# Kernel tuning notes

Measured on AMD Instinct MI355X. Metric: run time of the kernel, lower is better.

## Reference

```python
import jax, jax.numpy as jnp
import numpy as np

EPS = 1e-8
LAM = 1.0


def setup_inputs() -> dict:
    key = jax.random.key(0)
    k1, k2 = jax.random.split(key)
    B, H, W = 32, 512, 512
    output = jax.random.normal(k1, (B, 1, H, W), dtype=jnp.float32)
    target = jax.random.normal(k2, (B, 1, H, W), dtype=jnp.float32)
    return {"output": output, "target": target}


def _frc_loss(output, target):
    # squeeze channel dim: (B,1,H,W) -> (B,H,W)
    output = output[:, 0]
    target = target[:, 0]
    B, H, W = output.shape
    rnyquist = H // 2

    # radial index map (H,W): round(sqrt(fx^2 + fy^2)) in pixel-frequency units
    fx = jnp.fft.fftfreq(H, 1.0 / H)
    fy = jnp.fft.fftfreq(W, 1.0 / W)
    X, Y = jnp.meshgrid(fx, fy, indexing='ij')
    radial = jnp.round(jnp.sqrt(X ** 2 + Y ** 2)).astype(jnp.int32)
    # bins > rnyquist were ignored by the original loop -> dump into extra bin
    idx = jnp.where(radial > rnyquist, rnyquist + 1, radial).reshape(-1)  # (H*W,)

    F1 = jnp.fft.fft2(output, norm='forward')  # (B,H,W) complex
    F2 = jnp.fft.fft2(target, norm='forward')

    # per-pixel correlation terms, laid out (HW, B) for segment_sum over leading axis
    a = (F1.real * F2.real + F1.imag * F2.imag).reshape(B, -1).T
    b = (F1.imag * F2.real - F1.real * F2.imag).reshape(B, -1).T
    c1 = (F1.real ** 2 + F1.imag ** 2).reshape(B, -1).T
    c2 = (F2.real ** 2 + F2.imag ** 2).reshape(B, -1).T
    stacked = jnp.stack([a, b, c1, c2], axis=-1)  # (HW, B, 4)

    # single-pass radial-bin segment sum (replaces O(R*H*W) masked loop)
    sums = jax.ops.segment_sum(stacked, idx, num_segments=rnyquist + 2)
    sums = sums[:rnyquist + 1]  # drop overflow bin -> (rnyquist+1, B, 4)
    C_r, C_i, C1, C2 = sums[..., 0], sums[..., 1], sums[..., 2], sums[..., 3]

    frc = jnp.sqrt(C_r ** 2 + C_i ** 2) / (jnp.sqrt(C1 * C2) + EPS)
    return LAM * jnp.mean((1.0 - frc) ** 2)


def reference(output, target):
    return _frc_loss(output, target)
```

## Files before the change

### kernel.cpp

```cpp
#include <hip/hip_runtime.h>
#include <math.h>

#define NIMG 32
#define NB3  771
#define PI_F 3.14159265358979323846f

__device__ __forceinline__ float2 cadd(float2 a, float2 b){ return make_float2(a.x+b.x, a.y+b.y); }
__device__ __forceinline__ float2 csub(float2 a, float2 b){ return make_float2(a.x-b.x, a.y-b.y); }
__device__ __forceinline__ float2 cmul(float2 a, float2 b){ return make_float2(a.x*b.x - a.y*b.y, a.x*b.y + a.y*b.x); }
__device__ __forceinline__ float2 cmul_mi(float2 a){ return make_float2(a.y, -a.x); }
__device__ __forceinline__ float2 tw(const float2* T, int m){ return T[m + (m >> 3)]; }
__device__ __forceinline__ int   sw(int pos){ return pos + (pos >> 3); }

__device__ __forceinline__ void dft8(float2* x) {
    const float c = 0.70710678118654752f;
    float2 u0 = cadd(x[0], x[4]), u1 = cadd(x[1], x[5]);
    float2 u2 = cadd(x[2], x[6]), u3 = cadd(x[3], x[7]);
    float2 v0 = csub(x[0], x[4]);
    float2 d1 = csub(x[1], x[5]);
    float2 v1 = make_float2(c*(d1.x + d1.y), c*(d1.y - d1.x));
    float2 d2 = csub(x[2], x[6]);
    float2 v2 = make_float2(d2.y, -d2.x);
    float2 d3 = csub(x[3], x[7]);
    float2 v3 = make_float2(-c*(d3.x - d3.y), -c*(d3.x + d3.y));
    float2 e0 = cadd(u0,u2), e1 = cadd(u1,u3);
    float2 f0 = csub(u0,u2), f1 = cmul_mi(csub(u1,u3));
    float2 g0 = cadd(v0,v2), g1 = cadd(v1,v3);
    float2 h0 = csub(v0,v2), h1 = cmul_mi(csub(v1,v3));
    x[0] = cadd(e0,e1); x[4] = csub(e0,e1);
    x[2] = cadd(f0,f1); x[6] = csub(f0,f1);
    x[1] = cadd(g0,g1); x[5] = csub(g0,g1);
    x[3] = cadd(h0,h1); x[7] = csub(h0,h1);
}

__device__ __forceinline__ void wave_fft512_dual(float2* Xa, float2* Xb,
                                                 float2* Sw, const float2* T,
                                                 int J) {
    dft8(Xa);
    dft8(Xb);
#pragma unroll
    for (int k = 1; k < 8; ++k) Xa[k] = cmul(Xa[k], tw(T, J * k));
#pragma unroll
    for (int k = 1; k < 8; ++k) Xb[k] = cmul(Xb[k], tw(T, J * k));
    const int jj = J + (J >> 3);
    const int j2 = J & 7;
    const int bb = 72 * (J >> 3) + j2;

#pragma unroll
    for (int k = 0; k < 8; ++k) Sw[jj + 72*k] = Xa[k];
#pragma unroll
    for (int q = 0; q < 8; ++q) Xa[q] = Sw[bb + 9*q];
#pragma unroll
    for (int k = 0; k < 8; ++k) Sw[jj + 72*k] = Xb[k];
#pragma unroll
    for (int q = 0; q < 8; ++q) Xb[q] = Sw[bb + 9*q];

    dft8(Xa);
    dft8(Xb);
#pragma unroll
    for (int k = 1; k < 8; ++k) Xa[k] = cmul(Xa[k], tw(T, 8 * j2 * k));
#pragma unroll
    for (int k = 1; k < 8; ++k) Xb[k] = cmul(Xb[k], tw(T, 8 * j2 * k));

#pragma unroll
    for (int k = 0; k < 8; ++k) Sw[bb + 9*k] = Xa[k];
#pragma unroll
    for (int q = 0; q < 8; ++q) Xa[q] = Sw[9*J + q];
#pragma unroll
    for (int k = 0; k < 8; ++k) Sw[bb + 9*k] = Xb[k];
#pragma unroll
    for (int q = 0; q < 8; ++q) Xb[q] = Sw[9*J + q];

    dft8(Xa);
    dft8(Xb);
}

__global__ __launch_bounds__(256) void fft_rows_T(const float* __restrict__ xr,
                                                  const float* __restrict__ yr,
                                                  float2* __restrict__ Zt) {
    __shared__ float2 S[4 * 576];
    __shared__ float2 T[576];
    const int t = threadIdx.x, w = t >> 6, J = t & 63;
    const int im = blockIdx.x >> 6, grp = blockIdx.x & 63;

#pragma unroll
    for (int i = 0; i < 2; ++i) {
        const int m = t + 256 * i;
        float s, c;
        __sincosf(-2.0f * PI_F * (float)m / 512.0f, &s, &c);
        T[m + (m >> 3)] = make_float2(c, s);
    }

    const size_t b0 = ((size_t)(im * 512 + grp * 8 + w)) << 9;
    const size_t b1 = b0 + (4u << 9);
    float2 X0[8], X1[8];
#pragma unroll
    for (int q = 0; q < 8; ++q) {
        X0[q] = make_float2(xr[b0 + J + 64*q], yr[b0 + J + 64*q]);
        X1[q] = make_float2(xr[b1 + J + 64*q], yr[b1 + J + 64*q]);
    }
    __syncthreads();

    float2* Sw = S + w * 576;
    wave_fft512_dual(X0, X1, Sw, T, J);

    const int r = ((J & 7) << 3) | (J >> 3);

#pragma unroll
    for (int k = 0; k < 8; ++k) Sw[64*k + r] = X0[k];
    __syncthreads();
    float2 eA[4], eB[4];
#pragma unroll
    for (int j = 0; j < 4; ++j) { eA[j] = S[j*576 + t]; eB[j] = S[j*576 + t + 256]; }
    __syncthreads();

#pragma unroll
    for (int k = 0; k < 8; ++k) Sw[64*k + r] = X1[k];
    __syncthreads();

    const size_t zb = ((size_t)im << 18) + (grp << 3);
    {
        float4* o = (float4*)(Zt + zb + ((size_t)t << 9));
        float2 f0 = S[0*576 + t], f1 = S[1*576 + t];
        float2 f2 = S[2*576 + t], f3 = S[3*576 + t];
        o[0] = make_float4(eA[0].x, eA[0].y, eA[1].x, eA[1].y);
        o[1] = make_float4(eA[2].x, eA[2].y, eA[3].x, eA[3].y);
        o[2] = make_float4(f0.x, f0.y, f1.x, f1.y);
        o[3] = make_float4(f2.x, f2.y, f3.x, f3.y);
    }
    {
        float4* o = (float4*)(Zt + zb + ((size_t)(t + 256) << 9));
        float2 f0 = S[0*576 + t + 256], f1 = S[1*576 + t + 256];
        float2 f2 = S[2*576 + t + 256], f3 = S[3*576 + t + 256];
        o[0] = make_float4(eB[0].x, eB[0].y, eB[1].x, eB[1].y);
        o[1] = make_float4(eB[2].x, eB[2].y, eB[3].x, eB[3].y);
        o[2] = make_float4(f0.x, f0.y, f1.x, f1.y);
        o[3] = make_float4(f2.x, f2.y, f3.x, f3.y);
    }
}

__global__ __launch_bounds__(256) void fft_cols_rings(const float2* __restrict__ Zt,
                                                      float* __restrict__ sums,
                                                      int big) {
    __shared__ float2 S[4 * 576];
    __shared__ float2 T[576];
    __shared__ float  bins[258 * 3];
    const int t = threadIdx.x, w = t >> 6, J = t & 63;
    const int im = blockIdx.x >> 6, g = blockIdx.x & 63;
    const int p = 4 * g + w;

#pragma unroll
    for (int i = 0; i < 2; ++i) {
        const int m = t + 256 * i;
        float s, c;
        __sincosf(-2.0f * PI_F * (float)m / 512.0f, &s, &c);
        T[m + (m >> 3)] = make_float2(c, s);
    }
    for (int i = t; i < 258 * 3; i += 256) bins[i] = 0.0f;

    const int c0 = (p == 0) ? 0   : p;
    const int c1 = (p == 0) ? 256 : 512 - p;
    const float2* rp0 = Zt + ((size_t)im << 18) + ((size_t)c0 << 9);
    const float2* rp1 = Zt + ((size_t)im << 18) + ((size_t)c1 << 9);
    float2 X0[8], X1[8];
#pragma unroll
    for (int q = 0; q < 8; ++q) { X0[q] = rp0[J + 64*q]; X1[q] = rp1[J + 64*q]; }
    __syncthreads();

    float2* A = S + w * 576;
    const int r  = ((J & 7) << 3) | (J >> 3);
    const int pk = r + (r >> 3);

    const float scale = 1.0f / (512.0f * 512.0f);
    auto pix = [&](float2 zk, float2 zm, float& av, float& c1v, float& c2v) {
        float f1r = 0.5f * (zk.x + zm.x) * scale;
        float f1i = 0.5f * (zk.y - zm.y) * scale;
        float f2r = 0.5f * (zk.y + zm.y) * scale;
        float f2i = 0.5f * (zm.x - zk.x) * scale;
        av  = f1r * f2r + f1i * f2i;
        c1v = f1r * f1r + f1i * f1i;
        c2v = f2r * f2r + f2i * f2i;
    };
    auto flush = [&](int ring, float a, float b, float c) {
        if (ring >= 0 && ring <= 256) {
            unsafeAtomicAdd(&bins[ring*3+0], a);
            unsafeAtomicAdd(&bins[ring*3+1], b);
            unsafeAtomicAdd(&bins[ring*3+2], c);
        }
    };

    wave_fft512_dual(X0, X1, A, T, J);

#pragma unroll
    for (int k = 0; k < 8; ++k) A[72*k + pk] = X0[k];

    float2 asv[8];
    if (p == 0) {
        int cur0 = -1;
        float a0 = 0, b0 = 0, c0v = 0;
#pragma unroll
        for (int i = 0; i < 8; ++i) {
            const int ky  = 8*J + i;
            const int kyp = (512 - ky) & 511;
            float2 zk = A[sw(ky)], zm = A[sw(kyp)];
            const float fk = (ky < 256) ? (float)ky : (float)(ky - 512);
            float av, cv, dv;
            pix(zk, zm, av, cv, dv);
            int rr = (int)rintf(fabsf(fk)); if (rr > 256) rr = 257;
            if (rr != cur0) { flush(cur0, a0, b0, c0v); cur0 = rr; a0 = av; b0 = cv; c0v = dv; }
            else            { a0 += av; b0 += cv; c0v += dv; }
        }
        flush(cur0, a0, b0, c0v);
    } else {
#pragma unroll
        for (int i = 0; i < 8; ++i) asv[i] = A[9*J + i];
    }

#pragma unroll
    for (int k = 0; k < 8; ++k) A[72*k + pk] = X1[k];

    if (p == 0) {
        int cur1 = -1;
        float a1 = 0, b1 = 0, c1v = 0;
#pragma unroll
        for (int i = 0; i < 8; ++i) {
            const int ky  = 8*J + i;
            const int kyp = (512 - ky) & 511;
            float2 zk = A[sw(ky)], zm = A[sw(kyp)];
            const float fk = (ky < 256) ? (float)ky : (float)(ky - 512);
            float av, cv, dv;
            pix(zk, zm, av, cv, dv);
            int rr = (int)rintf(sqrtf(fk*fk + 65536.0f)); if (rr > 256) rr = 257;
            if (rr != cur1) { flush(cur1, a1, b1, c1v); cur1 = rr; a1 = av; b1 = cv; c1v = dv; }
            else            { a1 += av; b1 += cv; c1v += dv; }
        }
        flush(cur1, a1, b1, c1v);
    } else {
        const float fy2 = (float)p * (float)p;
        int curR = -1;
        float sA = 0, sB = 0, sC = 0;
#pragma unroll
        for (int i = 0; i < 8; ++i) {
            const int ky  = 8*J + i;
            const int kyp = (512 - ky) & 511;
            float2 zk = asv[i];
            float2 zm = A[sw(kyp)];
            float a1v, b1v, d1v, a2v, b2v, d2v;
            pix(zk, zm, a1v, b1v, d1v);
            pix(zm, zk, a2v, b2v, d2v);
            const float fk = (ky < 256) ? (float)ky : (float)(ky - 512);
            int rr = (int)rintf(sqrtf(fk*fk + fy2)); if (rr > 256) rr = 257;
            const float aa = a1v + a2v, bb = b1v + b2v, cc = d1v + d2v;
            if (rr != curR) { flush(curR, sA, sB, sC); curR = rr; sA = aa; sB = bb; sC = cc; }
            else            { sA += aa; sB += bb; sC += cc; }
        }
        flush(curR, sA, sB, sC);
    }
    __syncthreads();

    if (big) {
        float* dst = sums + (size_t)blockIdx.x * NB3;
        for (int i = t; i < NB3; i += 256) dst[i] = bins[i];
    } else {
        float* dst = sums + (size_t)(im * 8 + (g & 7)) * NB3;
        for (int i = t; i < NB3; i += 256) unsafeAtomicAdd(&dst[i], bins[i]);
    }
}

__global__ __launch_bounds__(256) void finalize(const float* __restrict__ sums,
                                                float* __restrict__ out, int spi) {
    const int b = blockIdx.x, t = threadIdx.x;
    float acc = 0.0f;
    for (int r = t; r < 257; r += 256) {
        float cr = 0.f, c1 = 0.f, c2 = 0.f;
        for (int s = 0; s < spi; ++s) {
            const float* pp = sums + (size_t)(b * spi + s) * NB3 + r * 3;
            cr += pp[0]; c1 += pp[1]; c2 += pp[2];
        }
        float frc = fabsf(cr) / (sqrtf(c1 * c2) + 1e-8f);
        float d = 1.0f - frc;
        acc += d * d;
    }
#pragma unroll
    for (int off = 32; off > 0; off >>= 1) acc += __shfl_down(acc, off);
    __shared__ float red[4];
    if ((t & 63) == 0) red[t >> 6] = acc;
    __syncthreads();
    if (t == 0)
        unsafeAtomicAdd(out, (red[0] + red[1] + red[2] + red[3]) *
                             (1.0f / (257.0f * (float)NIMG)));
}

extern "C" void kernel_launch(void* const* d_in, const int* in_sizes, int n_in,
                              void* d_out, int out_size, void* d_ws, size_t ws_size,
                              hipStream_t stream) {
    const float* xr = (const float*)d_in[0];
    const float* yr = (const float*)d_in[1];

    float2* Zt = (float2*)d_ws;
    const size_t ztBytes = ((size_t)NIMG << 18) * sizeof(float2);
    float* sums = (float*)((char*)d_ws + ztBytes);
    const int big = (ws_size >= ztBytes + (size_t)2048 * NB3 * sizeof(float)) ? 1 : 0;

    if (!big)
        hipMemsetAsync(sums, 0, (size_t)NIMG * 8 * NB3 * sizeof(float), stream);
    hipMemsetAsync(d_out, 0, sizeof(float), stream);

    fft_rows_T    <<<dim3(NIMG * 64), dim3(256), 0, stream>>>(xr, yr, Zt);
    fft_cols_rings<<<dim3(NIMG * 64), dim3(256), 0, stream>>>(Zt, sums, big);
    finalize      <<<dim3(NIMG), dim3(256), 0, stream>>>(sums, (float*)d_out, big ? 64 : 8);
}
```

Measured before the change: 207.3 us.

## Tile intermediate layout, fuse finalize via last-block reduction, drop memsets, use symmetry

The intermediate spectrum is now stored in 8-column tiles, so row-FFT stores and column-FFT loads use contiguous chunks instead of 4 KB-strided accesses. Zeroing of the partial sums and counter moves into the first kernel, which removes two memset launches. The finalize kernel is folded into the column kernel through an atomic counter, with the last block doing the final reduction. The mirrored pixel term is replaced by doubling the first, based on conjugate symmetry. Together these cut launch overhead and improve memory coalescing, at the cost of a serial tail reduction in one block and atomics on the partial sums.

```diff
diff --git a/kernel.cpp b/kernel.cpp
--- a/kernel.cpp
+++ b/kernel.cpp
@@ -3,6 +3,7 @@
 
 #define NIMG 32
 #define NB3  771
+#define NSLICE (NIMG * 8)
 #define PI_F 3.14159265358979323846f
 
 __device__ __forceinline__ float2 cadd(float2 a, float2 b){ return make_float2(a.x+b.x, a.y+b.y); }
@@ -77,11 +78,19 @@
 
 __global__ __launch_bounds__(256) void fft_rows_T(const float* __restrict__ xr,
                                                   const float* __restrict__ yr,
-                                                  float2* __restrict__ Zt) {
+                                                  float2* __restrict__ Zt,
+                                                  float* __restrict__ sums,
+                                                  unsigned int* __restrict__ counter) {
     __shared__ float2 S[4 * 576];
     __shared__ float2 T[576];
     const int t = threadIdx.x, w = t >> 6, J = t & 63;
     const int im = blockIdx.x >> 6, grp = blockIdx.x & 63;
+
+    if (blockIdx.x < NSLICE) {
+        float* z = sums + (size_t)blockIdx.x * NB3;
+        for (int i = t; i < NB3; i += 256) z[i] = 0.0f;
+        if (blockIdx.x == 0 && t == 0) *counter = 0u;
+    }
 
 #pragma unroll
     for (int i = 0; i < 2; ++i) {
@@ -118,9 +127,9 @@
     for (int k = 0; k < 8; ++k) Sw[64*k + r] = X1[k];
     __syncthreads();
 
-    const size_t zb = ((size_t)im << 18) + (grp << 3);
+    const size_t zb = ((size_t)im << 18) + ((size_t)grp << 12);
     {
-        float4* o = (float4*)(Zt + zb + ((size_t)t << 9));
+        float4* o = (float4*)(Zt + zb + ((size_t)t << 3));
         float2 f0 = S[0*576 + t], f1 = S[1*576 + t];
         float2 f2 = S[2*576 + t], f3 = S[3*576 + t];
         o[0] = make_float4(eA[0].x, eA[0].y, eA[1].x, eA[1].y);
@@ -129,7 +138,7 @@
         o[3] = make_float4(f2.x, f2.y, f3.x, f3.y);
     }
     {
-        float4* o = (float4*)(Zt + zb + ((size_t)(t + 256) << 9));
+        float4* o = (float4*)(Zt + zb + ((size_t)(t + 256) << 3));
         float2 f0 = S[0*576 + t + 256], f1 = S[1*576 + t + 256];
         float2 f2 = S[2*576 + t + 256], f3 = S[3*576 + t + 256];
         o[0] = make_float4(eB[0].x, eB[0].y, eB[1].x, eB[1].y);
@@ -141,10 +150,12 @@
 
 __global__ __launch_bounds__(256) void fft_cols_rings(const float2* __restrict__ Zt,
                                                       float* __restrict__ sums,
-                                                      int big) {
+                                                      unsigned int* __restrict__ counter,
+                                                      float* __restrict__ out) {
     __shared__ float2 S[4 * 576];
     __shared__ float2 T[576];
     __shared__ float  bins[258 * 3];
+    __shared__ int    lastFlag;
     const int t = threadIdx.x, w = t >> 6, J = t & 63;
     const int im = blockIdx.x >> 6, g = blockIdx.x & 63;
     const int p = 4 * g + w;
@@ -160,11 +171,17 @@
 
     const int c0 = (p == 0) ? 0   : p;
     const int c1 = (p == 0) ? 256 : 512 - p;
-    const float2* rp0 = Zt + ((size_t)im << 18) + ((size_t)c0 << 9);
-    const float2* rp1 = Zt + ((size_t)im << 18) + ((size_t)c1 << 9);
+    const size_t ibase = (size_t)im << 18;
+    const int lane8 = J & 7, hi8 = J >> 3;
+    const float2* q0 = Zt + ibase + ((size_t)c0 << 3) + lane8;
+    const float2* q1 = Zt + ibase + ((size_t)c1 << 3) + lane8;
     float2 X0[8], X1[8];
 #pragma unroll
-    for (int q = 0; q < 8; ++q) { X0[q] = rp0[J + 64*q]; X1[q] = rp1[J + 64*q]; }
+    for (int q = 0; q < 8; ++q) {
+        const size_t off = (size_t)(hi8 + 8*q) << 12;
+        X0[q] = q0[off];
+        X1[q] = q1[off];
+    }
     __syncthreads();
 
     float2* A = S + w * 576;
@@ -245,12 +262,11 @@
             const int kyp = (512 - ky) & 511;
             float2 zk = asv[i];
             float2 zm = A[sw(kyp)];
-            float a1v, b1v, d1v, a2v, b2v, d2v;
+            float a1v, b1v, d1v;
             pix(zk, zm, a1v, b1v, d1v);
-            pix(zm, zk, a2v, b2v, d2v);
             const float fk = (ky < 256) ? (float)ky : (float)(ky - 512);
             int rr = (int)rintf(sqrtf(fk*fk + fy2)); if (rr > 256) rr = 257;
-            const float aa = a1v + a2v, bb = b1v + b2v, cc = d1v + d2v;
+            const float aa = 2.0f*a1v, bb = 2.0f*b1v, cc = 2.0f*d1v;
             if (rr != curR) { flush(curR, sA, sB, sC); curR = rr; sA = aa; sB = bb; sC = cc; }
             else            { sA += aa; sB += bb; sC += cc; }
         }
@@ -258,37 +274,45 @@
     }
     __syncthreads();
 
-    if (big) {
-        float* dst = sums + (size_t)blockIdx.x * NB3;
-        for (int i = t; i < NB3; i += 256) dst[i] = bins[i];
-    } else {
+    {
         float* dst = sums + (size_t)(im * 8 + (g & 7)) * NB3;
         for (int i = t; i < NB3; i += 256) unsafeAtomicAdd(&dst[i], bins[i]);
     }
-}
-
-__global__ __launch_bounds__(256) void finalize(const float* __restrict__ sums,
-                                                float* __restrict__ out, int spi) {
-    const int b = blockIdx.x, t = threadIdx.x;
-    float acc = 0.0f;
-    for (int r = t; r < 257; r += 256) {
-        float cr = 0.f, c1 = 0.f, c2 = 0.f;
-        for (int s = 0; s < spi; ++s) {
-            const float* pp = sums + (size_t)(b * spi + s) * NB3 + r * 3;
-            cr += pp[0]; c1 += pp[1]; c2 += pp[2];
-        }
-        float frc = fabsf(cr) / (sqrtf(c1 * c2) + 1e-8f);
-        float d = 1.0f - frc;
-        acc += d * d;
-    }
-#pragma unroll
-    for (int off = 32; off > 0; off >>= 1) acc += __shfl_down(acc, off);
-    __shared__ float red[4];
-    if ((t & 63) == 0) red[t >> 6] = acc;
-    __syncthreads();
-    if (t == 0)
-        unsafeAtomicAdd(out, (red[0] + red[1] + red[2] + red[3]) *
-                             (1.0f / (257.0f * (float)NIMG)));
+
+    __syncthreads();
+    if (t == 0) {
+        __threadfence();
+        unsigned int old = atomicAdd(counter, 1u);
+        lastFlag = (old == (unsigned int)(gridDim.x - 1)) ? 1 : 0;
+    }
+    __syncthreads();
+    if (lastFlag) {
+        __threadfence();
+        float acc = 0.0f;
+        for (int idx = t; idx < NIMG * 257; idx += 256) {
+            const int imQ = idx / 257;
+            const int rr  = idx - imQ * 257;
+            const float* pp = sums + (size_t)imQ * 8 * NB3 + rr * 3;
+            float cr = 0.f, c1s = 0.f, c2s = 0.f;
+#pragma unroll
+            for (int s = 0; s < 8; ++s) {
+                cr  += pp[(size_t)s * NB3 + 0];
+                c1s += pp[(size_t)s * NB3 + 1];
+                c2s += pp[(size_t)s * NB3 + 2];
+            }
+            float frc = fabsf(cr) / (sqrtf(c1s * c2s) + 1e-8f);
+            float d = 1.0f - frc;
+            acc += d * d;
+        }
+#pragma unroll
+        for (int off = 32; off > 0; off >>= 1) acc += __shfl_down(acc, off);
+        __shared__ float red[4];
+        if ((t & 63) == 0) red[t >> 6] = acc;
+        __syncthreads();
+        if (t == 0)
+            out[0] = (red[0] + red[1] + red[2] + red[3]) *
+                     (1.0f / (257.0f * (float)NIMG));
+    }
 }
 
 extern "C" void kernel_launch(void* const* d_in, const int* in_sizes, int n_in,
@@ -300,13 +324,9 @@
     float2* Zt = (float2*)d_ws;
     const size_t ztBytes = ((size_t)NIMG << 18) * sizeof(float2);
     float* sums = (float*)((char*)d_ws + ztBytes);
-    const int big = (ws_size >= ztBytes + (size_t)2048 * NB3 * sizeof(float)) ? 1 : 0;
-
-    if (!big)
-        hipMemsetAsync(sums, 0, (size_t)NIMG * 8 * NB3 * sizeof(float), stream);
-    hipMemsetAsync(d_out, 0, sizeof(float), stream);
-
-    fft_rows_T    <<<dim3(NIMG * 64), dim3(256), 0, stream>>>(xr, yr, Zt);
-    fft_cols_rings<<<dim3(NIMG * 64), dim3(256), 0, stream>>>(Zt, sums, big);
-    finalize      <<<dim3(NIMG), dim3(256), 0, stream>>>(sums, (float*)d_out, big ? 64 : 8);
-}
+    unsigned int* counter = (unsigned int*)((char*)d_ws + ztBytes +
+                              (size_t)NSLICE * NB3 * sizeof(float));
+
+    fft_rows_T    <<<dim3(NIMG * 64), dim3(256), 0, stream>>>(xr, yr, Zt, sums, counter);
+    fft_cols_rings<<<dim3(NIMG * 64), dim3(256), 0, stream>>>(Zt, sums, counter, (float*)d_out);
+}
```

Result: faster. 202.1 us (-2.5%).
